# Kernel tuning notes

Measured on AMD Instinct MI355X. Metric: run time of the kernel, lower is better.

The kernel has to match this reference:

```python
import jax, jax.numpy as jnp
import numpy as np

HEADS = 16
D_MODEL = 1024
D_EXP = 2048  # d_model * expansion_factor
D_HEAD = D_EXP // HEADS
DEPTH = 12
B, L = 2, 2048


def setup_inputs() -> dict:
    key = jax.random.key(0)
    ks = jax.random.split(key, 4)
    x = jax.random.normal(ks[0], (B, L, D_MODEL), dtype=jnp.float32)
    w_in = jax.random.normal(ks[1], (4 * D_EXP, D_MODEL), dtype=jnp.float32) * 0.02
    w_out = jax.random.normal(ks[2], (D_MODEL, D_EXP), dtype=jnp.float32) * (0.02 / np.sqrt(2 * DEPTH))
    # LearnedALiBi init: logspace(0,-6,heads//2,base=2) ++ zeros(heads - heads//2)
    half = HEADS // 2
    slopes = jnp.concatenate([
        jnp.asarray(2.0 ** np.linspace(0.0, -6.0, half), dtype=jnp.float32),
        jnp.zeros((HEADS - half,), dtype=jnp.float32),
    ])
    smear_factor = jnp.linspace(-6.0, 6.0, HEADS, dtype=jnp.float32)
    return {
        "x": x, "w_in": w_in, "w_out": w_out,
        "ln_in_g": jnp.ones((D_MODEL,), jnp.float32), "ln_in_b": jnp.zeros((D_MODEL,), jnp.float32),
        "ln_out_g": jnp.ones((D_MODEL,), jnp.float32), "ln_out_b": jnp.zeros((D_MODEL,), jnp.float32),
        "slopes": slopes, "smear_factor": smear_factor,
    }


def _layernorm(x, g, b, eps=1e-5):
    mu = jnp.mean(x, axis=-1, keepdims=True)
    var = jnp.mean(jnp.square(x - mu), axis=-1, keepdims=True)
    return (x - mu) * jax.lax.rsqrt(var + eps) * g + b


def reference(x, w_in, w_out, ln_in_g, ln_in_b, ln_out_g, ln_out_b, slopes, smear_factor):
    b, l, d = x.shape
    h = _layernorm(x, ln_in_g, ln_in_b)
    qkvp = h @ w_in.T  # (b, l, 4*D_EXP)
    q, k, v, p = jnp.split(qkvp, 4, axis=-1)

    def to_heads(t):  # b i (h d) -> b h i d
        return t.reshape(b, l, HEADS, D_HEAD).transpose(0, 2, 1, 3)

    q, k, v = to_heads(q), to_heads(k), to_heads(v)

    # key smearing: k_i <- (1-s)*k_i + s*k_{i-1}
    smear = jax.nn.sigmoid(smear_factor)[None, :, None, None]
    k_shift = jnp.pad(k, ((0, 0), (0, 0), (1, 0), (0, 0)))[:, :, :-1]
    k = (1.0 - smear) * k + smear * k_shift

    logits = jnp.einsum('bhid,bhjd->bhij', q, k) * (D_HEAD ** -0.5)
    # learned ALiBi bias: j * slope_h  (depends only on key index)
    alibi = jnp.arange(l, dtype=logits.dtype)[None, None, None, :] * slopes[None, :, None, None]
    # causal bias: -1e10 * (1 - tril)
    i_idx = jnp.arange(l)
    causal = jnp.where(i_idx[:, None] >= i_idx[None, :], 0.0, -1e10)[None, None]
    a = jax.nn.softmax(logits + alibi + causal, axis=-1)

    o = jnp.einsum('bhij,bhjd->bhid', a, v)
    o = o.transpose(0, 2, 1, 3).reshape(b, l, D_EXP)  # b h i d -> b i (h d)
    gated = jax.nn.silu(p) * o
    y = gated @ w_out.T
    return _layernorm(y, ln_out_g, ln_out_b)
```

## Files before the change

### kernel.cpp

```cpp
#include <hip/hip_runtime.h>
#include <hip/hip_bf16.h>
#include <stdint.h>


typedef __bf16 bf16;
typedef bf16  bf16x8 __attribute__((ext_vector_type(8)));
typedef bf16  bf16x4 __attribute__((ext_vector_type(4)));
typedef float f32x4  __attribute__((ext_vector_type(4)));

#define SEQ   2048
#define NBATC 2

__device__ __forceinline__ void gld_lds16(const bf16* g, bf16* l) {
  __builtin_amdgcn_global_load_lds((const __attribute__((address_space(1))) void*)g,
                                   (__attribute__((address_space(3))) void*)l, 16, 0, 0);
}

__global__ __launch_bounds__(256) void cvt_kernel(const float* __restrict__ in,
                                                  bf16* __restrict__ out, int n8) {
  int t = blockIdx.x * 256 + threadIdx.x;
  if (t >= n8) return;
  const float4* p = (const float4*)in + (size_t)t * 2;
  float4 a = p[0], b = p[1];
  bf16x8 o;
  o[0] = (bf16)a.x; o[1] = (bf16)a.y; o[2] = (bf16)a.z; o[3] = (bf16)a.w;
  o[4] = (bf16)b.x; o[5] = (bf16)b.y; o[6] = (bf16)b.z; o[7] = (bf16)b.w;
  *((bf16x8*)out + t) = o;
}

template<bool BF16OUT>
__global__ __launch_bounds__(256) void ln_kernel(const float* __restrict__ x,
    const float* __restrict__ gamma, const float* __restrict__ beta,
    void* __restrict__ out) {
  const int row = blockIdx.x;
  const int tid = threadIdx.x;
  float4 v = *(const float4*)(x + (size_t)row * 1024 + tid * 4);
  float s  = v.x + v.y + v.z + v.w;
  float ss = v.x * v.x + v.y * v.y + v.z * v.z + v.w * v.w;
#pragma unroll
  for (int m = 1; m < 64; m <<= 1) { s += __shfl_xor(s, m, 64); ss += __shfl_xor(ss, m, 64); }
  __shared__ float red[8];
  if ((tid & 63) == 0) { red[tid >> 6] = s; red[(tid >> 6) + 4] = ss; }
  __syncthreads();
  s  = red[0] + red[1] + red[2] + red[3];
  ss = red[4] + red[5] + red[6] + red[7];
  const float mu  = s * (1.f / 1024.f);
  const float inv = rsqrtf(ss * (1.f / 1024.f) - mu * mu + 1e-5f);
  float4 g  = *(const float4*)(gamma + tid * 4);
  float4 bb = *(const float4*)(beta  + tid * 4);
  float y0 = (v.x - mu) * inv * g.x + bb.x;
  float y1 = (v.y - mu) * inv * g.y + bb.y;
  float y2 = (v.z - mu) * inv * g.z + bb.z;
  float y3 = (v.w - mu) * inv * g.w + bb.w;
  if (BF16OUT) {
    bf16* o = (bf16*)out + (size_t)row * 1024 + tid * 4;
    o[0] = (bf16)y0; o[1] = (bf16)y1; o[2] = (bf16)y2; o[3] = (bf16)y3;
  } else {
    float* o = (float*)out + (size_t)row * 1024 + tid * 4;
    o[0] = y0; o[1] = y1; o[2] = y2; o[3] = y3;
  }
}

__global__ __launch_bounds__(256) void prep_kernel(const bf16* __restrict__ qkvp,
    const float* __restrict__ smf, bf16* __restrict__ ksm, bf16* __restrict__ vt) {
  __shared__ bf16 T[128][72];
  const int kt = blockIdx.x, bh = blockIdx.y;
  const int b = bh >> 4, h = bh & 15;
  const int t = threadIdx.x;

  {
    int i = t >> 2, d0 = (t & 3) * 32;
    const bf16* src = qkvp + (size_t)(b * SEQ + kt * 64 + i) * 8192 + 4096 + h * 128 + d0;
#pragma unroll
    for (int m = 0; m < 4; m++) {
      bf16x8 v8 = *(const bf16x8*)(src + m * 8);
#pragma unroll
      for (int e = 0; e < 8; e++) T[d0 + m * 8 + e][i] = v8[e];
    }
  }

  {
    float sm = 1.f / (1.f + __expf(-smf[h]));
#pragma unroll
    for (int j = 0; j < 4; j++) {
      int c  = j * 256 + t;
      int il = c >> 4, d8 = c & 15;
      int i  = kt * 64 + il;
      const bf16* base = qkvp + (size_t)(b * SEQ + i) * 8192 + 2048 + h * 128 + d8 * 8;
      bf16x8 cur = *(const bf16x8*)base;
      bf16x8 prv = cur;
      if (i > 0) prv = *(const bf16x8*)(base - 8192);
      bf16x8 o;
#pragma unroll
      for (int e = 0; e < 8; e++) {
        float pv = (i > 0) ? (float)prv[e] : 0.f;
        o[e] = (bf16)((1.f - sm) * (float)cur[e] + sm * pv);
      }
      size_t idx = ((size_t)bh * SEQ + i) * 128 + ((d8 * 8) ^ ((i & 7) << 3));
      *(bf16x8*)(ksm + idx) = o;
    }
  }

  __syncthreads();
  {
    int d = t >> 1, i0 = (t & 1) * 32;
    bf16* dst = vt + (size_t)bh * (SEQ * 128) + (size_t)kt * 8192 + d * 64;
#pragma unroll
    for (int m = 0; m < 4; m++) {
      bf16x8 v8 = *(const bf16x8*)&T[d][i0 + m * 8];
      *(bf16x8*)(dst + (((i0 + m * 8)) ^ ((d & 7) << 3))) = v8;
    }
  }
}

__global__ __launch_bounds__(512) void gemm256(const bf16* __restrict__ A,
    const bf16* __restrict__ Bt, bf16* __restrict__ C, int M, int N, int K,
    int RX, int SX, int SY) {
  __shared__ bf16 As[2][256 * 64];
  __shared__ bf16 Bs[2][256 * 64];
  const int w   = blockIdx.x;
  const int xcd = w & 7, idx = w >> 3;
  const int rx = xcd % RX, ry = xcd / RX;
  const int bx = rx * SX + idx % SX;
  const int by = ry * SY + idx / SX;
  const int tid  = threadIdx.x;
  const int lane = tid & 63, wid = tid >> 6;
  const int l4 = lane >> 4, l16 = lane & 15;
  const int wr = wid >> 2, wc = wid & 3;
  const int rowBase = by * 256, colBase = bx * 256;
  const int NT = K >> 6;

  f32x4 acc[8][4];
  const f32x4 z = {0.f, 0.f, 0.f, 0.f};
#pragma unroll
  for (int i = 0; i < 8; i++)
#pragma unroll
    for (int j = 0; j < 4; j++) acc[i][j] = z;

  auto stage = [&](int kt, int bsel) {
    const int k0 = kt * 64;
    bf16* ad = &As[bsel][tid * 8];
    bf16* bd = &Bs[bsel][tid * 8];
#pragma unroll
    for (int j = 0; j < 4; ++j) {
      const int c   = j * 512 + tid;
      const int row = c >> 3;
      const int sc  = ((c & 7) * 8) ^ ((row & 7) << 3);
      gld_lds16(A  + (size_t)(rowBase + row) * K + k0 + sc, ad + j * 4096);
      gld_lds16(Bt + (size_t)(colBase + row) * K + k0 + sc, bd + j * 4096);
    }
  };

  stage(0, 0);
  for (int t = 0; t < NT; ++t) {
    const int cur = t & 1;
    if (t + 1 < NT) {
      stage(t + 1, cur ^ 1);
      asm volatile("s_waitcnt vmcnt(8)" ::: "memory");
    } else {
      asm volatile("s_waitcnt vmcnt(0)" ::: "memory");
    }
    asm volatile("s_barrier" ::: "memory");
    const bf16* a_ = &As[cur][0];
    const bf16* b_ = &Bs[cur][0];
#pragma unroll
    for (int ks = 0; ks < 2; ++ks) {
      bf16x8 bfr[4];
#pragma unroll
      for (int ni = 0; ni < 4; ++ni) {
        const int br = wc * 64 + ni * 16 + l16;
        bfr[ni] = *(const bf16x8*)&b_[br * 64 + ((ks * 32 + l4 * 8) ^ ((br & 7) << 3))];
      }
#pragma unroll
      for (int mi = 0; mi < 8; ++mi) {
        const int ar = wr * 128 + mi * 16 + l16;
        bf16x8 af = *(const bf16x8*)&a_[ar * 64 + ((ks * 32 + l4 * 8) ^ ((ar & 7) << 3))];
#pragma unroll
        for (int ni = 0; ni < 4; ++ni)
          acc[mi][ni] = __builtin_amdgcn_mfma_f32_16x16x32_bf16(af, bfr[ni], acc[mi][ni], 0, 0, 0);
      }
    }
    asm volatile("s_waitcnt lgkmcnt(0)" ::: "memory");
    asm volatile("s_barrier" ::: "memory");
  }

#pragma unroll
  for (int mi = 0; mi < 8; ++mi)
#pragma unroll
    for (int ni = 0; ni < 4; ++ni) {
      int row = rowBase + wr * 128 + mi * 16 + l4 * 4;
      int col = colBase + wc * 64 + ni * 16 + l16;
#pragma unroll
      for (int r = 0; r < 4; ++r)
        C[(size_t)(row + r) * N + col] = (bf16)acc[mi][ni][r];
    }
}

template<typename OutT>
__global__ __launch_bounds__(256) void gemm_bt(const bf16* __restrict__ A,
    const bf16* __restrict__ Bt, OutT* __restrict__ C, int M, int N, int K,
    int RX, int SX, int SY) {
  __shared__ bf16 As[128 * 32];
  __shared__ bf16 Bs[128 * 32];
  const int w   = blockIdx.x;
  const int xcd = w & 7, idx = w >> 3;
  const int rx = xcd % RX, ry = xcd / RX;
  const int bx = rx * SX + idx % SX;
  const int by = ry * SY + idx / SX;
  const int tid  = threadIdx.x;
  const int lane = tid & 63, wid = tid >> 6;
  const int l4 = lane >> 4, l16 = lane & 15;
  const int wr = wid >> 1, wc = wid & 1;
  const int rowBase = by * 128, colBase = bx * 128;

  const bf16* gA = A  + (size_t)(rowBase + (tid >> 2)) * K + (tid & 3) * 8;
  const bf16* gB = Bt + (size_t)(colBase + (tid >> 2)) * K + (tid & 3) * 8;
  const size_t rowStep = (size_t)64 * K;

  f32x4 acc[4][4];
  const f32x4 z = {0.f, 0.f, 0.f, 0.f};
#pragma unroll
  for (int i = 0; i < 4; i++)
#pragma unroll
    for (int j = 0; j < 4; j++) acc[i][j] = z;

  for (int k0 = 0; k0 < K; k0 += 32) {
    __syncthreads();
    gld_lds16(gA + k0,           &As[tid * 8]);
    gld_lds16(gA + rowStep + k0, &As[2048 + tid * 8]);
    gld_lds16(gB + k0,           &Bs[tid * 8]);
    gld_lds16(gB + rowStep + k0, &Bs[2048 + tid * 8]);
    __syncthreads();
    bf16x8 af[4], bfr[4];
#pragma unroll
    for (int mi = 0; mi < 4; mi++)
      af[mi] = *(const bf16x8*)&As[(wr * 64 + mi * 16 + l16) * 32 + l4 * 8];
#pragma unroll
    for (int ni = 0; ni < 4; ni++)
      bfr[ni] = *(const bf16x8*)&Bs[(wc * 64 + ni * 16 + l16) * 32 + l4 * 8];
#pragma unroll
    for (int mi = 0; mi < 4; mi++)
#pragma unroll
      for (int ni = 0; ni < 4; ni++)
        acc[mi][ni] = __builtin_amdgcn_mfma_f32_16x16x32_bf16(af[mi], bfr[ni], acc[mi][ni], 0, 0, 0);
  }
#pragma unroll
  for (int mi = 0; mi < 4; mi++)
#pragma unroll
    for (int ni = 0; ni < 4; ni++) {
      int row = rowBase + wr * 64 + mi * 16 + l4 * 4;
      int col = colBase + wc * 64 + ni * 16 + l16;
#pragma unroll
      for (int r = 0; r < 4; r++)
        C[(size_t)(row + r) * N + col] = (OutT)acc[mi][ni][r];
    }
}

__global__ __launch_bounds__(512, 2) void attn_kernel(const bf16* __restrict__ qkvp,
    const bf16* __restrict__ ksm, const bf16* __restrict__ vt,
    const float* __restrict__ slopes, bf16* __restrict__ gated) {
  const int w   = blockIdx.x;
  const int xcd = w & 7;
  const int bh  = xcd * 4 + ((w >> 3) & 3);
  const int pr  = w >> 5;
  const int b   = bh >> 4, h = bh & 15;
  const int tid = threadIdx.x, wid = tid >> 6, lane = tid & 63;
  const int l4 = lane >> 4, l16 = lane & 15;
  const int swz = (l16 & 7) << 3;
  const float LOG2E = 1.44269504f;
  const float s2 = 0.08838834764831845f * LOG2E;
  const float slopeL = slopes[h] * LOG2E;

  __shared__ bf16 Kb[4][64 * 128];
  __shared__ bf16 Vb[4][64 * 128];
  __shared__ bf16 P_lds[128 * 64];

  const bf16* ksmB = ksm + (size_t)bh * SEQ * 128;
  const bf16* vtB  = vt  + (size_t)bh * SEQ * 128;

  auto stage = [&](int kt, int bsel) {
#pragma unroll
    for (int j = 0; j < 2; j++) {
      const int c = j * 512 + tid;
      gld_lds16(ksmB + (size_t)kt * 8192 + c * 8, &Kb[bsel][c * 8]);
      gld_lds16(vtB  + (size_t)kt * 8192 + c * 8, &Vb[bsel][c * 8]);
    }
  };

  auto run_strip = [&](int qtile) {
    const int nt = 2 * qtile + 2;
    const int iq = qtile * 128 + wid * 16 + l16;
    bf16x8 qf[4];
    {
      const bf16* qrow = qkvp + (size_t)(b * SEQ + iq) * 8192 + h * 128;
#pragma unroll
      for (int kb = 0; kb < 4; kb++) qf[kb] = *(const bf16x8*)(qrow + kb * 32 + l4 * 8);
    }
    f32x4 oacc[8];
    const f32x4 z = {0.f, 0.f, 0.f, 0.f};
#pragma unroll
    for (int i = 0; i < 8; i++) oacc[i] = z;
    float m2 = -1e38f, lpart = 0.f;

    auto tile = [&](int t, const bf16* K_, const bf16* V_) {
      f32x4 sacc[4];
#pragma unroll
      for (int jf = 0; jf < 4; jf++) {
        f32x4 a = z;
#pragma unroll
        for (int kb = 0; kb < 4; kb++) {
          bf16x8 kf = *(const bf16x8*)&K_[(jf * 16 + l16) * 128 + ((kb * 32 + l4 * 8) ^ swz)];
          a = __builtin_amdgcn_mfma_f32_16x16x32_bf16(kf, qf[kb], a, 0, 0, 0);
        }
        sacc[jf] = a;
      }

      const bool diag = (t >= 2 * qtile);
      const int kbase = t * 64 + l4 * 4;
#pragma unroll
      for (int jf = 0; jf < 4; jf++) {
#pragma unroll
        for (int r = 0; r < 4; r++) {
          int j = kbase + jf * 16 + r;
          float v = fmaf(sacc[jf][r], s2, (float)j * slopeL);
          if (diag && j > iq) v = -1e38f;
          sacc[jf][r] = v;
        }
      }

      float mx = sacc[0][0];
#pragma unroll
      for (int jf = 0; jf < 4; jf++)
#pragma unroll
        for (int r = 0; r < 4; r++) mx = fmaxf(mx, sacc[jf][r]);
      mx = fmaxf(mx, __shfl_xor(mx, 16, 64));
      mx = fmaxf(mx, __shfl_xor(mx, 32, 64));

      if (__any(mx > m2 + 14.f)) {
        float mnew  = fmaxf(m2, mx);
        float alpha = __builtin_amdgcn_exp2f(m2 - mnew);
        m2 = mnew;
        lpart *= alpha;
#pragma unroll
        for (int df = 0; df < 8; df++) oacc[df] *= alpha;
      }

      float rs = 0.f;
#pragma unroll
      for (int jf = 0; jf < 4; jf++) {
        bf16x4 pw;
#pragma unroll
        for (int r = 0; r < 4; r++) {
          float pe = __builtin_amdgcn_exp2f(sacc[jf][r] - m2);
          rs += pe;
          pw[r] = (bf16)pe;
        }
        *(bf16x4*)&P_lds[(wid * 16 + l16) * 64 + ((jf * 16 + l4 * 4) ^ swz)] = pw;
      }
      lpart += rs;

#pragma unroll
      for (int kb2 = 0; kb2 < 2; ++kb2) {
        bf16x8 pf = *(const bf16x8*)&P_lds[(wid * 16 + l16) * 64 + ((kb2 * 32 + l4 * 8) ^ swz)];
#pragma unroll
        for (int df = 0; df < 8; df++) {
          bf16x8 vf = *(const bf16x8*)&V_[(df * 16 + l16) * 64 + ((kb2 * 32 + l4 * 8) ^ swz)];
          oacc[df] = __builtin_amdgcn_mfma_f32_16x16x32_bf16(vf, pf, oacc[df], 0, 0, 0);
        }
      }
    };

    stage(0, 0);
    stage(1, 1);
    for (int tp = 0; tp < nt; tp += 2) {
      if (tp + 2 < nt) {
        stage(tp + 2, (tp + 2) & 3);
        stage(tp + 3, (tp + 3) & 3);
        asm volatile("s_waitcnt vmcnt(8)" ::: "memory");
      } else {
        asm volatile("s_waitcnt vmcnt(0)" ::: "memory");
      }
      __builtin_amdgcn_sched_barrier(0);
      __builtin_amdgcn_s_barrier();
      tile(tp,     Kb[tp & 3],       Vb[tp & 3]);
      tile(tp + 1, Kb[(tp + 1) & 3], Vb[(tp + 1) & 3]);
      asm volatile("s_waitcnt lgkmcnt(0)" ::: "memory");
      __builtin_amdgcn_s_barrier();
    }

    lpart += __shfl_xor(lpart, 16, 64);
    lpart += __shfl_xor(lpart, 32, 64);
    const float linv = 1.f / lpart;
    const bf16* pgrow = qkvp + (size_t)(b * SEQ + iq) * 8192 + 6144 + h * 128;
    bf16* grow = gated + (size_t)(b * SEQ + iq) * 2048 + h * 128;
#pragma unroll
    for (int df = 0; df < 8; df++) {
      const int d0 = df * 16 + l4 * 4;
      bf16x4 pg4 = *(const bf16x4*)(pgrow + d0);
      bf16x4 o4;
#pragma unroll
      for (int r = 0; r < 4; r++) {
        float o  = oacc[df][r] * linv;
        float pg = (float)pg4[r];
        float silu = pg / (1.f + __expf(-pg));
        o4[r] = (bf16)(silu * o);
      }
      *(bf16x4*)(grow + d0) = o4;
    }
  };

  run_strip(15 - pr);
  run_strip(pr);
}

extern "C" void kernel_launch(void* const* d_in, const int* in_sizes, int n_in,
                              void* d_out, int out_size, void* d_ws, size_t ws_size,
                              hipStream_t stream) {
  (void)in_sizes; (void)n_in; (void)out_size; (void)ws_size;
  const float* x      = (const float*)d_in[0];
  const float* w_in   = (const float*)d_in[1];
  const float* w_out  = (const float*)d_in[2];
  const float* lnig   = (const float*)d_in[3];
  const float* lnib   = (const float*)d_in[4];
  const float* lnog   = (const float*)d_in[5];
  const float* lnob   = (const float*)d_in[6];
  const float* slopes = (const float*)d_in[7];
  const float* smf    = (const float*)d_in[8];
  float* out = (float*)d_out;

  char* ws = (char*)d_ws;
  size_t off = 0;
  bf16* hb      = (bf16*)(ws + off); off += (size_t)4096 * 1024 * 2;
  bf16* w_in_b  = (bf16*)(ws + off); off += (size_t)8192 * 1024 * 2;
  bf16* w_out_b = (bf16*)(ws + off); off += (size_t)1024 * 2048 * 2;
  bf16* qkvp    = (bf16*)(ws + off); off += (size_t)4096 * 8192 * 2;
  bf16* ksm     = (bf16*)(ws + off); off += (size_t)32 * 2048 * 128 * 2;
  bf16* gated   = (bf16*)(ws + off); off += (size_t)4096 * 2048 * 2;
  float* yb     = (float*)(ws + off); off += (size_t)4096 * 1024 * 4;
  bf16* vt      = (bf16*)yb;

  cvt_kernel<<<4096, 256, 0, stream>>>(w_in,  w_in_b,  8388608 / 8);
  cvt_kernel<<<1024, 256, 0, stream>>>(w_out, w_out_b, 2097152 / 8);
  ln_kernel<true><<<4096, 256, 0, stream>>>(x, lnig, lnib, hb);
  gemm256<<<512, 512, 0, stream>>>(hb, w_in_b, qkvp, 4096, 8192, 1024, 4, 8, 8);
  prep_kernel<<<dim3(32, 32), 256, 0, stream>>>(qkvp, smf, ksm, vt);
  attn_kernel<<<256, 512, 0, stream>>>(qkvp, ksm, vt, slopes, gated);
  gemm_bt<float><<<256, 256, 0, stream>>>(gated, w_out_b, yb, 4096, 1024, 2048, 1, 8, 4);
  ln_kernel<false><<<4096, 256, 0, stream>>>(yb, lnog, lnob, out);
}
```

Baseline: 230.4 us.

## Restructure 256-tile GEMM main loop into four phased sub-steps with interleaved prefetch

The gemm256 main loop is split into four phases per k-tile. Each phase loads a quarter of the A fragments from LDS, issues the next tile's global-to-LDS copies spread across phases, raises wave priority around the MFMA block, and synchronises with barriers. The LDS buffers are reorganised into 128-row halves, and launch bounds request two blocks per CU. The aim is to overlap global loads, LDS reads and MFMA more finely, at the cost of more barriers per iteration and more register pressure from the occupancy hint.

Result: no change. 229.1 us (-0.6%).

```diff
diff --git a/kernel.cpp b/kernel.cpp
--- a/kernel.cpp
+++ b/kernel.cpp
@@ -113,11 +113,11 @@
   }
 }
 
-__global__ __launch_bounds__(512) void gemm256(const bf16* __restrict__ A,
+__global__ __launch_bounds__(512, 2) void gemm256(const bf16* __restrict__ A,
     const bf16* __restrict__ Bt, bf16* __restrict__ C, int M, int N, int K,
     int RX, int SX, int SY) {
-  __shared__ bf16 As[2][256 * 64];
-  __shared__ bf16 Bs[2][256 * 64];
+  __shared__ bf16 As[2][2][128 * 64];
+  __shared__ bf16 Bs[2][2][128 * 64];
   const int w   = blockIdx.x;
   const int xcd = w & 7, idx = w >> 3;
   const int rx = xcd % RX, ry = xcd / RX;
@@ -137,51 +137,69 @@
 #pragma unroll
     for (int j = 0; j < 4; j++) acc[i][j] = z;
 
-  auto stage = [&](int kt, int bsel) {
-    const int k0 = kt * 64;
-    bf16* ad = &As[bsel][tid * 8];
-    bf16* bd = &Bs[bsel][tid * 8];
-#pragma unroll
-    for (int j = 0; j < 4; ++j) {
-      const int c   = j * 512 + tid;
-      const int row = c >> 3;
-      const int sc  = ((c & 7) * 8) ^ ((row & 7) << 3);
-      gld_lds16(A  + (size_t)(rowBase + row) * K + k0 + sc, ad + j * 4096);
-      gld_lds16(Bt + (size_t)(colBase + row) * K + k0 + sc, bd + j * 4096);
+  auto stage_pair = [&](int t_, int hp) {
+    const int buf = t_ & 1, k0 = t_ * 64;
+#pragma unroll
+    for (int half = 0; half < 2; ++half) {
+      const bf16* src = (hp == 0) ? (A  + (size_t)(rowBase + half * 128) * K)
+                                  : (Bt + (size_t)(colBase + half * 128) * K);
+      bf16* dst = (hp == 0) ? &As[buf][half][0] : &Bs[buf][half][0];
+#pragma unroll
+      for (int j = 0; j < 2; ++j) {
+        const int c   = j * 512 + tid;
+        const int row = c >> 3;
+        const int sc  = ((c & 7) * 8) ^ ((row & 7) << 3);
+        gld_lds16(src + (size_t)row * K + k0 + sc, dst + c * 8);
+      }
     }
   };
 
-  stage(0, 0);
+  stage_pair(0, 0);
+  stage_pair(0, 1);
+  asm volatile("s_waitcnt vmcnt(0)" ::: "memory");
+  __builtin_amdgcn_sched_barrier(0);
+  __builtin_amdgcn_s_barrier();
+
   for (int t = 0; t < NT; ++t) {
-    const int cur = t & 1;
-    if (t + 1 < NT) {
-      stage(t + 1, cur ^ 1);
-      asm volatile("s_waitcnt vmcnt(8)" ::: "memory");
-    } else {
-      asm volatile("s_waitcnt vmcnt(0)" ::: "memory");
-    }
-    asm volatile("s_barrier" ::: "memory");
-    const bf16* a_ = &As[cur][0];
-    const bf16* b_ = &Bs[cur][0];
-#pragma unroll
-    for (int ks = 0; ks < 2; ++ks) {
-      bf16x8 bfr[4];
-#pragma unroll
-      for (int ni = 0; ni < 4; ++ni) {
-        const int br = wc * 64 + ni * 16 + l16;
-        bfr[ni] = *(const bf16x8*)&b_[br * 64 + ((ks * 32 + l4 * 8) ^ ((br & 7) << 3))];
-      }
-#pragma unroll
-      for (int mi = 0; mi < 8; ++mi) {
-        const int ar = wr * 128 + mi * 16 + l16;
-        bf16x8 af = *(const bf16x8*)&a_[ar * 64 + ((ks * 32 + l4 * 8) ^ ((ar & 7) << 3))];
+    const int buf = t & 1;
+    const bf16* aH = &As[buf][wr][0];
+    const bf16* bH = &Bs[buf][wc >> 1][0];
+    bf16x8 bfr[4];
+#pragma unroll
+    for (int p = 0; p < 4; ++p) {
+      const int ks = p >> 1, mh = p & 1;
+      bf16x8 af[4];
+#pragma unroll
+      for (int q = 0; q < 4; ++q) {
+        const int lr = mh * 64 + q * 16 + l16;
+        af[q] = *(const bf16x8*)&aH[lr * 64 + ((ks * 32 + l4 * 8) ^ ((lr & 7) << 3))];
+      }
+      if (mh == 0) {
+#pragma unroll
+        for (int ni = 0; ni < 4; ++ni) {
+          const int lr = (wc & 1) * 64 + ni * 16 + l16;
+          bfr[ni] = *(const bf16x8*)&bH[lr * 64 + ((ks * 32 + l4 * 8) ^ ((lr & 7) << 3))];
+        }
+      }
+      if (p == 0 && t + 1 < NT) stage_pair(t + 1, 0);
+      if (p == 1 && t + 1 < NT) stage_pair(t + 1, 1);
+      __builtin_amdgcn_s_barrier();
+      asm volatile("s_waitcnt lgkmcnt(0)" ::: "memory");
+      __builtin_amdgcn_sched_barrier(0);
+      __builtin_amdgcn_s_setprio(1);
+#pragma unroll
+      for (int q = 0; q < 4; ++q)
 #pragma unroll
         for (int ni = 0; ni < 4; ++ni)
-          acc[mi][ni] = __builtin_amdgcn_mfma_f32_16x16x32_bf16(af, bfr[ni], acc[mi][ni], 0, 0, 0);
-      }
-    }
-    asm volatile("s_waitcnt lgkmcnt(0)" ::: "memory");
-    asm volatile("s_barrier" ::: "memory");
+          acc[mh * 4 + q][ni] =
+              __builtin_amdgcn_mfma_f32_16x16x32_bf16(af[q], bfr[ni], acc[mh * 4 + q][ni], 0, 0, 0);
+      __builtin_amdgcn_s_setprio(0);
+      if (p == 3) {
+        asm volatile("s_waitcnt vmcnt(0)" ::: "memory");
+        __builtin_amdgcn_sched_barrier(0);
+      }
+      __builtin_amdgcn_s_barrier();
+    }
   }
 
 #pragma unroll
```
